# Performance work log

Measured on AMD Instinct MI355X. Metric: run time of the kernel, lower is better.

Reference implementation:

```python
import jax, jax.numpy as jnp
import numpy as np

EPS = 1e-5  # BatchNorm eps (eval mode, uses running stats)


def _conv1x1(x, W, b):
    # x: [B,C,H,W], W: [O,C], b: [O] -> [B,O,H,W]
    return jnp.einsum('bchw,oc->bohw', x, W) + b[None, :, None, None]


def setup_inputs() -> dict:
    key = jax.random.key(0)
    ks = jax.random.split(key, 13)
    B, C, M, N = 16, 512, 64, 64
    CR = C // 2
    s = 0.02
    return {
        'x': jax.random.normal(ks[0], (B, C, M, N), dtype=jnp.float32),
        'Wq': jax.random.normal(ks[1], (CR, C), dtype=jnp.float32) * s,
        'bq': jax.random.normal(ks[2], (CR,), dtype=jnp.float32) * s,
        'Wk': jax.random.normal(ks[3], (CR, C), dtype=jnp.float32) * s,
        'bk': jax.random.normal(ks[4], (CR,), dtype=jnp.float32) * s,
        'Wv': jax.random.normal(ks[5], (CR, C), dtype=jnp.float32) * s,
        'bv': jax.random.normal(ks[6], (CR,), dtype=jnp.float32) * s,
        'Wr': jax.random.normal(ks[7], (C, CR), dtype=jnp.float32) * s,
        'br': jax.random.normal(ks[8], (C,), dtype=jnp.float32) * s,
        'gamma': jax.random.normal(ks[9], (C,), dtype=jnp.float32) * 0.1 + 1.0,
        'beta': jax.random.normal(ks[10], (C,), dtype=jnp.float32) * 0.1,
        'running_mean': jax.random.normal(ks[11], (C,), dtype=jnp.float32) * 0.1,
        'running_var': jax.random.uniform(ks[12], (C,), dtype=jnp.float32, minval=0.5, maxval=1.5),
    }


def reference(x, Wq, bq, Wk, bk, Wv, bv, Wr, br, gamma, beta, running_mean, running_var):
    b, c, m, n = x.shape
    cr = Wq.shape[0]
    # 1x1-conv QKV projections
    Q = _conv1x1(x, Wq, bq).reshape(b * cr, m, n)
    K = _conv1x1(x, Wk, bk).reshape(b * cr, m, n)
    V = _conv1x1(x, Wv, bv).reshape(b * cr, m, n)
    # per-channel spatial attention over rows: [b*cr, m, m]
    corr = jnp.einsum('gik,gjk->gij', Q, K)
    attn = jax.nn.softmax(corr, axis=-1)
    y = jnp.einsum('gij,gjn->gin', attn, V).reshape(b, cr, m, n)
    # reconstruct: 1x1 conv + BatchNorm (eval mode) + residual
    y = _conv1x1(y, Wr, br)
    inv = gamma / jnp.sqrt(running_var + EPS)
    y = y * inv[None, :, None, None] + (beta - running_mean * inv)[None, :, None, None]
    return y + x
```

## Files before the change

### kernel.cpp

```cpp
#include <hip/hip_runtime.h>

typedef __attribute__((ext_vector_type(8))) short bf16x8;
typedef __attribute__((ext_vector_type(4))) float f32x4;

#define DEVI static __device__ __forceinline__

DEVI unsigned short f2b(float f) {
  union { float f; unsigned u; } v; v.f = f;
  unsigned r = v.u + 0x7fffu + ((v.u >> 16) & 1u);
  return (unsigned short)(r >> 16);
}

typedef const __attribute__((address_space(1))) void* gas1_t;
typedef __attribute__((address_space(3))) void* las3_t;
#define GL16(g, l) __builtin_amdgcn_global_load_lds((gas1_t)(g), (las3_t)(l), 16, 0, 0)

#define WAITVM(N) asm volatile("s_waitcnt vmcnt(" #N ")" ::: "memory")
#define WAITLGKM  asm volatile("s_waitcnt lgkmcnt(0)" ::: "memory")
#define SCHEDBAR  __builtin_amdgcn_sched_barrier(0)

#define OFF_WQKV  0ull
#define OFF_WR    786432ull
#define OFF_BQKV  1048576ull
#define OFF_SCALE 1051648ull
#define OFF_OFF2  1053696ull
#define OFF_XT    2097152ull
#define OFF_YT    2097152ull
#define OFF_Y     35651584ull
#define OFF_Q     69206016ull

__global__ __launch_bounds__(256) void k_xt(
    const float* __restrict__ x, unsigned short* __restrict__ xt,
    const float* __restrict__ Wq, const float* __restrict__ bq,
    const float* __restrict__ Wk, const float* __restrict__ bk,
    const float* __restrict__ Wv, const float* __restrict__ bv,
    const float* __restrict__ Wr, const float* __restrict__ br,
    const float* __restrict__ gamma, const float* __restrict__ beta,
    const float* __restrict__ rm, const float* __restrict__ rv,
    unsigned short* __restrict__ wqkv, unsigned short* __restrict__ wrb,
    float* __restrict__ bqkv, float* __restrict__ scale, float* __restrict__ off2)
{
  __shared__ unsigned short tile[64][72];
  const int t = threadIdx.x;
  const int bid = blockIdx.x + blockIdx.y * 64 + blockIdx.z * 512;

  if (bid < 1536) {
    int i = bid * 256 + t;
    if (i < 768 * 512) {
      int o = i >> 9, c = i & 511;
      float v = (o < 256) ? Wq[o * 512 + c] : (o < 512 ? Wk[(o - 256) * 512 + c] : Wv[(o - 512) * 512 + c]);
      wqkv[i] = f2b(v);
    }
    if (i < 512 * 256) wrb[i] = f2b(Wr[i]);
    if (i < 768) bqkv[i] = (i < 256) ? bq[i] : (i < 512 ? bk[i - 256] : bv[i - 512]);
    if (i < 512) {
      float inv = gamma[i] * rsqrtf(rv[i] + 1e-5f);
      scale[i] = inv;
      off2[i] = (br[i] - rm[i]) * inv + beta[i];
    }
  }

  const int b = blockIdx.z, c0 = blockIdx.y * 64, s0 = blockIdx.x * 64;
  const int r = t >> 2, cc = (t & 3) * 16;
  const float* src = x + ((size_t)b * 512 + c0 + r) * 4096 + s0 + cc;
  #pragma unroll
  for (int j = 0; j < 16; j += 4) {
    float4 v = *(const float4*)(src + j);
    tile[r][cc + j + 0] = f2b(v.x);
    tile[r][cc + j + 1] = f2b(v.y);
    tile[r][cc + j + 2] = f2b(v.z);
    tile[r][cc + j + 3] = f2b(v.w);
  }
  __syncthreads();
  unsigned short* dst = xt + ((size_t)b * 4096 + s0 + r) * 512 + c0 + cc;
  bf16x8 o0, o1;
  #pragma unroll
  for (int j = 0; j < 8; ++j) { o0[j] = tile[cc + j][r]; o1[j] = tile[cc + 8 + j][r]; }
  *(bf16x8*)(dst) = o0;
  *(bf16x8*)(dst + 8) = o1;
}

__global__ __launch_bounds__(512, 2) void k_qkv(
    const unsigned short* __restrict__ xt, const unsigned short* __restrict__ wqkv,
    const float* __restrict__ bqkv, unsigned short* __restrict__ qkv)
{
  __shared__ unsigned short Ab[2][16384];
  __shared__ unsigned short Bb[2][16384];
  const int b = blockIdx.z, o0 = blockIdx.y * 256, s0 = blockIdx.x * 256;
  const int t = threadIdx.x, w = t >> 6, l = t & 63;
  const int wm = w >> 2, wn = w & 3, lr = l & 15;
  const int lkE = (l >> 4) * 8;
  const int swE = (lr & 7) * 8;
  const int cp = (t & 7) ^ ((t >> 3) & 7);

  const unsigned short* Ag = wqkv + (size_t)(o0 + (t >> 3)) * 512 + cp * 8;
  const unsigned short* Bg = xt + ((size_t)b * 4096 + s0 + (t >> 3)) * 512 + cp * 8;

  const f32x4 z = {0.f, 0.f, 0.f, 0.f};
  f32x4 acc[8][4];
  #pragma unroll
  for (int i = 0; i < 8; ++i)
    #pragma unroll
    for (int j = 0; j < 4; ++j) acc[i][j] = z;

#define STG4(bn, kt, ph) do { \
    GL16(Ag + (kt) * 64 + (size_t)(2 * (ph) + 0) * 64 * 512, (char*)&Ab[bn][0] + (2 * (ph) + 0) * 8192 + t * 16); \
    GL16(Ag + (kt) * 64 + (size_t)(2 * (ph) + 1) * 64 * 512, (char*)&Ab[bn][0] + (2 * (ph) + 1) * 8192 + t * 16); \
    GL16(Bg + (kt) * 64 + (size_t)(2 * (ph) + 0) * 64 * 512, (char*)&Bb[bn][0] + (2 * (ph) + 0) * 8192 + t * 16); \
    GL16(Bg + (kt) * 64 + (size_t)(2 * (ph) + 1) * 64 * 512, (char*)&Bb[bn][0] + (2 * (ph) + 1) * 8192 + t * 16); \
  } while (0)

  bf16x8 af[2][4];
#define PHASE(bn, mh, nh, LOADA) do { \
    bf16x8 bfr[2][2]; \
    _Pragma("unroll") \
    for (int kc = 0; kc < 2; ++kc) { \
      const int kidx = (kc * 32 + lkE) ^ swE; \
      if (LOADA) { \
        _Pragma("unroll") \
        for (int mi4 = 0; mi4 < 4; ++mi4) \
          af[kc][mi4] = *(const bf16x8*)(&Ab[bn][(wm * 128 + ((mh) * 4 + mi4) * 16 + lr) * 64 + kidx]); \
      } \
      _Pragma("unroll") \
      for (int ni2 = 0; ni2 < 2; ++ni2) \
        bfr[kc][ni2] = *(const bf16x8*)(&Bb[bn][(wn * 64 + ((nh) * 2 + ni2) * 16 + lr) * 64 + kidx]); \
    } \
    WAITLGKM; SCHEDBAR; \
    __builtin_amdgcn_s_setprio(1); \
    _Pragma("unroll") \
    for (int kc = 0; kc < 2; ++kc) \
      _Pragma("unroll") \
      for (int mi4 = 0; mi4 < 4; ++mi4) \
        _Pragma("unroll") \
        for (int ni2 = 0; ni2 < 2; ++ni2) \
          acc[(mh) * 4 + mi4][(nh) * 2 + ni2] = \
            __builtin_amdgcn_mfma_f32_16x16x32_bf16(af[kc][mi4], bfr[kc][ni2], acc[(mh) * 4 + mi4][(nh) * 2 + ni2], 0, 0, 0); \
    __builtin_amdgcn_s_setprio(0); \
  } while (0)

  STG4(0, 0, 0); STG4(0, 0, 1);
  #pragma unroll
  for (int kt = 0; kt < 8; ++kt) {
    const int bn = kt & 1;
    if (kt < 7) STG4(bn ^ 1, kt + 1, 0);
    if (kt == 7) { WAITVM(0); } else { WAITVM(4); }
    __builtin_amdgcn_s_barrier(); SCHEDBAR;
    PHASE(bn, 0, 0, 1);
    __builtin_amdgcn_s_barrier(); SCHEDBAR;
    if (kt < 7) STG4(bn ^ 1, kt + 1, 1);
    PHASE(bn, 0, 1, 0);
    __builtin_amdgcn_s_barrier(); SCHEDBAR;
    PHASE(bn, 1, 0, 1);
    __builtin_amdgcn_s_barrier(); SCHEDBAR;
    PHASE(bn, 1, 1, 0);
    __builtin_amdgcn_s_barrier(); SCHEDBAR;
  }

  #pragma unroll
  for (int mi = 0; mi < 8; ++mi) {
    #pragma unroll
    for (int reg = 0; reg < 4; ++reg) {
      const int o = o0 + wm * 128 + mi * 16 + (l >> 4) * 4 + reg;
      const float bias = bqkv[o];
      const size_t base = (size_t)(o >> 8) * 16777216ull + ((size_t)b * 256 + (o & 255)) * 4096;
      #pragma unroll
      for (int ni = 0; ni < 4; ++ni) {
        const int s = s0 + wn * 64 + ni * 16 + lr;
        qkv[base + s] = f2b(acc[mi][ni][reg] + bias);
      }
    }
  }
#undef STG4
#undef PHASE
}

__global__ __launch_bounds__(256) void k_attn(const unsigned short* __restrict__ qkv,
                                              unsigned short* __restrict__ yout)
{
  __shared__ unsigned short Vt[64][80];
  __shared__ unsigned short P[4][16][80];
  const int g = blockIdx.x;
  const unsigned short* qg = qkv + (size_t)g * 4096;
  const unsigned short* kg = qkv + 16777216ull + (size_t)g * 4096;
  const unsigned short* vg = qkv + 33554432ull + (size_t)g * 4096;
  const int t = threadIdx.x, w = t >> 6, l = t & 63;
  const int lr = l & 15, lk = (l >> 4) * 8;

  {
    const int j = t >> 2, c0 = (t & 3) * 16;
    bf16x8 a = *(const bf16x8*)(vg + j * 64 + c0);
    bf16x8 bb = *(const bf16x8*)(vg + j * 64 + c0 + 8);
    #pragma unroll
    for (int jj = 0; jj < 8; ++jj) { Vt[c0 + jj][j] = a[jj]; Vt[c0 + 8 + jj][j] = bb[jj]; }
  }

  const f32x4 z = {0.f, 0.f, 0.f, 0.f};
  bf16x8 qf[2];
  #pragma unroll
  for (int kc = 0; kc < 2; ++kc) qf[kc] = *(const bf16x8*)(qg + (w * 16 + lr) * 64 + kc * 32 + lk);
  f32x4 accS[4] = {z, z, z, z};
  __builtin_amdgcn_s_setprio(1);
  #pragma unroll
  for (int jt = 0; jt < 4; ++jt)
    #pragma unroll
    for (int kc = 0; kc < 2; ++kc) {
      bf16x8 kf = *(const bf16x8*)(kg + (jt * 16 + lr) * 64 + kc * 32 + lk);
      accS[jt] = __builtin_amdgcn_mfma_f32_16x16x32_bf16(qf[kc], kf, accS[jt], 0, 0, 0);
    }
  __builtin_amdgcn_s_setprio(0);

  #pragma unroll
  for (int reg = 0; reg < 4; ++reg) {
    float mx = fmaxf(fmaxf(accS[0][reg], accS[1][reg]), fmaxf(accS[2][reg], accS[3][reg]));
    #pragma unroll
    for (int m = 1; m < 16; m <<= 1) mx = fmaxf(mx, __shfl_xor(mx, m, 64));
    float e0 = __expf(accS[0][reg] - mx), e1 = __expf(accS[1][reg] - mx);
    float e2 = __expf(accS[2][reg] - mx), e3 = __expf(accS[3][reg] - mx);
    float sm = e0 + e1 + e2 + e3;
    #pragma unroll
    for (int m = 1; m < 16; m <<= 1) sm += __shfl_xor(sm, m, 64);
    const float rs = 1.f / sm;
    const int row = (l >> 4) * 4 + reg;
    P[w][row][0 * 16 + lr] = f2b(e0 * rs);
    P[w][row][1 * 16 + lr] = f2b(e1 * rs);
    P[w][row][2 * 16 + lr] = f2b(e2 * rs);
    P[w][row][3 * 16 + lr] = f2b(e3 * rs);
  }
  __syncthreads();

  bf16x8 pf[2];
  #pragma unroll
  for (int kc = 0; kc < 2; ++kc) pf[kc] = *(const bf16x8*)(&P[w][lr][kc * 32 + lk]);
  f32x4 accY[4] = {z, z, z, z};
  __builtin_amdgcn_s_setprio(1);
  #pragma unroll
  for (int nt = 0; nt < 4; ++nt)
    #pragma unroll
    for (int kc = 0; kc < 2; ++kc) {
      bf16x8 vf = *(const bf16x8*)(&Vt[nt * 16 + lr][kc * 32 + lk]);
      accY[nt] = __builtin_amdgcn_mfma_f32_16x16x32_bf16(pf[kc], vf, accY[nt], 0, 0, 0);
    }
  __builtin_amdgcn_s_setprio(0);

  unsigned short* yg = yout + (size_t)g * 4096;
  #pragma unroll
  for (int nt = 0; nt < 4; ++nt)
    #pragma unroll
    for (int reg = 0; reg < 4; ++reg) {
      const int i = w * 16 + (l >> 4) * 4 + reg;
      yg[i * 64 + nt * 16 + lr] = f2b(accY[nt][reg]);
    }
}

__global__ __launch_bounds__(256) void k_yt(const unsigned short* __restrict__ y, unsigned short* __restrict__ yt)
{
  __shared__ unsigned short tile[64][72];
  const int b = blockIdx.z, cr0 = blockIdx.y * 64, s0 = blockIdx.x * 64;
  const int t = threadIdx.x, r = t >> 2, c0 = (t & 3) * 16;
  const unsigned short* src = y + ((size_t)b * 256 + cr0 + r) * 4096 + s0 + c0;
  bf16x8 a = *(const bf16x8*)(src);
  bf16x8 bb = *(const bf16x8*)(src + 8);
  #pragma unroll
  for (int j = 0; j < 8; ++j) { tile[r][c0 + j] = a[j]; tile[r][c0 + 8 + j] = bb[j]; }
  __syncthreads();
  unsigned short* dst = yt + ((size_t)b * 4096 + s0 + r) * 256 + cr0 + c0;
  bf16x8 o0, o1;
  #pragma unroll
  for (int j = 0; j < 8; ++j) { o0[j] = tile[c0 + j][r]; o1[j] = tile[c0 + 8 + j][r]; }
  *(bf16x8*)(dst) = o0;
  *(bf16x8*)(dst + 8) = o1;
}

__global__ __launch_bounds__(256) void k_recon(
    const unsigned short* __restrict__ yt, const unsigned short* __restrict__ wrb,
    const float* __restrict__ scale, const float* __restrict__ off2,
    const float* __restrict__ x, float* __restrict__ out)
{
  __shared__ unsigned short lds[2][2][8192];
  const int b = blockIdx.z, o0 = blockIdx.y * 128, s0 = blockIdx.x * 128;
  const int t = threadIdx.x, w = t >> 6, l = t & 63;
  const int wm = w >> 1, wn = w & 1, lr = l & 15;
  const int lkE = (l >> 4) * 8;
  const int swE = (lr & 7) * 8;
  const int cp = (t & 7) ^ ((t >> 3) & 7);

  const unsigned short* Ag = wrb + (size_t)(o0 + (t >> 3)) * 256 + cp * 8;
  const unsigned short* Bg = yt + ((size_t)b * 4096 + s0 + (t >> 3)) * 256 + cp * 8;

  const f32x4 z = {0.f, 0.f, 0.f, 0.f};
  f32x4 acc[4][4];
  #pragma unroll
  for (int i = 0; i < 4; ++i)
    #pragma unroll
    for (int j = 0; j < 4; ++j) acc[i][j] = z;

#define STG_R(st, kt) do { \
    _Pragma("unroll") \
    for (int j = 0; j < 4; ++j) { \
      GL16(Ag + (kt) * 64 + j * 32 * 256, (char*)&lds[st][0][0] + j * 4096 + t * 16); \
      GL16(Bg + (kt) * 64 + j * 32 * 256, (char*)&lds[st][1][0] + j * 4096 + t * 16); \
    } \
  } while (0)

#define CMP_R(st) do { \
    const unsigned short* A  = &lds[st][0][0]; \
    const unsigned short* Bl = &lds[st][1][0]; \
    _Pragma("unroll") \
    for (int kc = 0; kc < 2; ++kc) { \
      const int kidx = (kc * 32 + lkE) ^ swE; \
      bf16x8 af[4], bfr[4]; \
      _Pragma("unroll") \
      for (int mi = 0; mi < 4; ++mi) af[mi] = *(const bf16x8*)(A + (wm * 64 + mi * 16 + lr) * 64 + kidx); \
      _Pragma("unroll") \
      for (int ni = 0; ni < 4; ++ni) bfr[ni] = *(const bf16x8*)(Bl + (wn * 64 + ni * 16 + lr) * 64 + kidx); \
      _Pragma("unroll") \
      for (int mi = 0; mi < 4; ++mi) \
        _Pragma("unroll") \
        for (int ni = 0; ni < 4; ++ni) \
          acc[mi][ni] = __builtin_amdgcn_mfma_f32_16x16x32_bf16(af[mi], bfr[ni], acc[mi][ni], 0, 0, 0); \
    } \
    WAITLGKM; SCHEDBAR; \
  } while (0)

  STG_R(0, 0); STG_R(1, 1);
  #pragma unroll
  for (int kt = 0; kt < 3; ++kt) {
    WAITVM(8);
    __builtin_amdgcn_s_barrier(); SCHEDBAR;
    CMP_R(kt & 1);
    __builtin_amdgcn_s_barrier(); SCHEDBAR;
    if (kt + 2 < 4) STG_R(kt & 1, kt + 2);
  }
  WAITVM(0);
  __builtin_amdgcn_s_barrier(); SCHEDBAR;
  CMP_R(1);

  #pragma unroll
  for (int mi = 0; mi < 4; ++mi) {
    #pragma unroll
    for (int reg = 0; reg < 4; ++reg) {
      const int o = o0 + wm * 64 + mi * 16 + (l >> 4) * 4 + reg;
      const float sc = scale[o], of = off2[o];
      const size_t base = ((size_t)b * 512 + o) * 4096;
      #pragma unroll
      for (int ni = 0; ni < 4; ++ni) {
        const int s = s0 + wn * 64 + ni * 16 + lr;
        const size_t idx = base + s;
        out[idx] = acc[mi][ni][reg] * sc + of + x[idx];
      }
    }
  }
#undef STG_R
#undef CMP_R
}

extern "C" void kernel_launch(void* const* d_in, const int* in_sizes, int n_in,
                              void* d_out, int out_size, void* d_ws, size_t ws_size,
                              hipStream_t stream)
{
  const float* x     = (const float*)d_in[0];
  const float* Wq    = (const float*)d_in[1];
  const float* bq    = (const float*)d_in[2];
  const float* Wk    = (const float*)d_in[3];
  const float* bk    = (const float*)d_in[4];
  const float* Wv    = (const float*)d_in[5];
  const float* bv    = (const float*)d_in[6];
  const float* Wr    = (const float*)d_in[7];
  const float* br    = (const float*)d_in[8];
  const float* gamma = (const float*)d_in[9];
  const float* beta  = (const float*)d_in[10];
  const float* rm    = (const float*)d_in[11];
  const float* rv    = (const float*)d_in[12];

  char* ws = (char*)d_ws;
  unsigned short* wqkv  = (unsigned short*)(ws + OFF_WQKV);
  unsigned short* wrb   = (unsigned short*)(ws + OFF_WR);
  float* bqkv  = (float*)(ws + OFF_BQKV);
  float* scale = (float*)(ws + OFF_SCALE);
  float* off2  = (float*)(ws + OFF_OFF2);
  unsigned short* xt  = (unsigned short*)(ws + OFF_XT);
  unsigned short* yt  = (unsigned short*)(ws + OFF_YT);
  unsigned short* yb  = (unsigned short*)(ws + OFF_Y);
  unsigned short* qkv = (unsigned short*)(ws + OFF_Q);
  float* out = (float*)d_out;

  hipLaunchKernelGGL(k_xt, dim3(64, 8, 16), dim3(256), 0, stream,
                     x, xt, Wq, bq, Wk, bk, Wv, bv, Wr, br, gamma, beta, rm, rv,
                     wqkv, wrb, bqkv, scale, off2);
  hipLaunchKernelGGL(k_qkv, dim3(16, 3, 16), dim3(512), 0, stream, xt, wqkv, bqkv, qkv);
  hipLaunchKernelGGL(k_attn, dim3(4096), dim3(256), 0, stream, qkv, yb);
  hipLaunchKernelGGL(k_yt, dim3(64, 4, 16), dim3(256), 0, stream, yb, yt);
  hipLaunchKernelGGL(k_recon, dim3(32, 4, 16), dim3(256), 0, stream, yt, wrb, scale, off2, x, out);
}
```

Baseline: 219.8 us.

## Split QKV GEMM staging into four quarter-loads and restructure LDS-read/MFMA phases

The QKV projection GEMM main loop now issues the next tile's global-to-LDS loads in four smaller groups spread across the four compute phases instead of two larger groups. Its LDS fragment reads are split from the MFMA blocks, with extra barriers between them, so that loads and MFMA work interleave more finely. The reconstruct GEMM's inner step now reads both k-chunks of fragments before issuing all MFMAs and drops the trailing lgkm wait. The aim is better overlap of memory traffic with matrix math. The cost is more barriers per iteration and higher register pressure.

```diff
diff --git a/kernel.cpp b/kernel.cpp
--- a/kernel.cpp
+++ b/kernel.cpp
@@ -103,28 +103,40 @@
     #pragma unroll
     for (int j = 0; j < 4; ++j) acc[i][j] = z;
 
-#define STG4(bn, kt, ph) do { \
-    GL16(Ag + (kt) * 64 + (size_t)(2 * (ph) + 0) * 64 * 512, (char*)&Ab[bn][0] + (2 * (ph) + 0) * 8192 + t * 16); \
-    GL16(Ag + (kt) * 64 + (size_t)(2 * (ph) + 1) * 64 * 512, (char*)&Ab[bn][0] + (2 * (ph) + 1) * 8192 + t * 16); \
-    GL16(Bg + (kt) * 64 + (size_t)(2 * (ph) + 0) * 64 * 512, (char*)&Bb[bn][0] + (2 * (ph) + 0) * 8192 + t * 16); \
-    GL16(Bg + (kt) * 64 + (size_t)(2 * (ph) + 1) * 64 * 512, (char*)&Bb[bn][0] + (2 * (ph) + 1) * 8192 + t * 16); \
+#define STG2(bn, kt, h) do { \
+    const int c0_ = ((h) & 1) * 2, c1_ = c0_ + 1; \
+    if ((h) < 2) { \
+      GL16(Ag + (kt) * 64 + (size_t)c0_ * 64 * 512, (char*)&Ab[bn][0] + c0_ * 8192 + t * 16); \
+      GL16(Ag + (kt) * 64 + (size_t)c1_ * 64 * 512, (char*)&Ab[bn][0] + c1_ * 8192 + t * 16); \
+    } else { \
+      GL16(Bg + (kt) * 64 + (size_t)c0_ * 64 * 512, (char*)&Bb[bn][0] + c0_ * 8192 + t * 16); \
+      GL16(Bg + (kt) * 64 + (size_t)c1_ * 64 * 512, (char*)&Bb[bn][0] + c1_ * 8192 + t * 16); \
+    } \
   } while (0)
 
   bf16x8 af[2][4];
-#define PHASE(bn, mh, nh, LOADA) do { \
-    bf16x8 bfr[2][2]; \
+
+#define READ_A(bn, mh) do { \
     _Pragma("unroll") \
     for (int kc = 0; kc < 2; ++kc) { \
       const int kidx = (kc * 32 + lkE) ^ swE; \
-      if (LOADA) { \
-        _Pragma("unroll") \
-        for (int mi4 = 0; mi4 < 4; ++mi4) \
-          af[kc][mi4] = *(const bf16x8*)(&Ab[bn][(wm * 128 + ((mh) * 4 + mi4) * 16 + lr) * 64 + kidx]); \
-      } \
+      _Pragma("unroll") \
+      for (int mi4 = 0; mi4 < 4; ++mi4) \
+        af[kc][mi4] = *(const bf16x8*)(&Ab[bn][(wm * 128 + ((mh) * 4 + mi4) * 16 + lr) * 64 + kidx]); \
+    } \
+  } while (0)
+
+#define READ_B(bn, nh, bfr) do { \
+    _Pragma("unroll") \
+    for (int kc = 0; kc < 2; ++kc) { \
+      const int kidx = (kc * 32 + lkE) ^ swE; \
       _Pragma("unroll") \
       for (int ni2 = 0; ni2 < 2; ++ni2) \
         bfr[kc][ni2] = *(const bf16x8*)(&Bb[bn][(wn * 64 + ((nh) * 2 + ni2) * 16 + lr) * 64 + kidx]); \
     } \
+  } while (0)
+
+#define MFMA_Q(mh, nh, bfr) do { \
     WAITLGKM; SCHEDBAR; \
     __builtin_amdgcn_s_setprio(1); \
     _Pragma("unroll") \
@@ -138,21 +150,32 @@
     __builtin_amdgcn_s_setprio(0); \
   } while (0)
 
-  STG4(0, 0, 0); STG4(0, 0, 1);
+  STG2(0, 0, 0); STG2(0, 0, 1); STG2(0, 0, 2); STG2(0, 0, 3);
+
   #pragma unroll
   for (int kt = 0; kt < 8; ++kt) {
     const int bn = kt & 1;
-    if (kt < 7) STG4(bn ^ 1, kt + 1, 0);
-    if (kt == 7) { WAITVM(0); } else { WAITVM(4); }
-    __builtin_amdgcn_s_barrier(); SCHEDBAR;
-    PHASE(bn, 0, 0, 1);
-    __builtin_amdgcn_s_barrier(); SCHEDBAR;
-    if (kt < 7) STG4(bn ^ 1, kt + 1, 1);
-    PHASE(bn, 0, 1, 0);
-    __builtin_amdgcn_s_barrier(); SCHEDBAR;
-    PHASE(bn, 1, 0, 1);
-    __builtin_amdgcn_s_barrier(); SCHEDBAR;
-    PHASE(bn, 1, 1, 0);
+    bf16x8 bfr[2][2];
+    if (kt < 7) STG2(bn ^ 1, kt + 1, 0);
+    if (kt == 7) { WAITVM(0); } else { WAITVM(2); }
+    __builtin_amdgcn_s_barrier(); SCHEDBAR;
+    READ_A(bn, 0); READ_B(bn, 0, bfr); SCHEDBAR;
+    MFMA_Q(0, 0, bfr);
+    __builtin_amdgcn_s_barrier(); SCHEDBAR;
+    READ_B(bn, 1, bfr); SCHEDBAR;
+    if (kt < 7) STG2(bn ^ 1, kt + 1, 1);
+    __builtin_amdgcn_s_barrier(); SCHEDBAR;
+    MFMA_Q(0, 1, bfr);
+    __builtin_amdgcn_s_barrier(); SCHEDBAR;
+    READ_A(bn, 1); READ_B(bn, 0, bfr); SCHEDBAR;
+    if (kt < 7) STG2(bn ^ 1, kt + 1, 2);
+    __builtin_amdgcn_s_barrier(); SCHEDBAR;
+    MFMA_Q(1, 0, bfr);
+    __builtin_amdgcn_s_barrier(); SCHEDBAR;
+    READ_B(bn, 1, bfr); SCHEDBAR;
+    if (kt < 7) STG2(bn ^ 1, kt + 1, 3);
+    __builtin_amdgcn_s_barrier(); SCHEDBAR;
+    MFMA_Q(1, 1, bfr);
     __builtin_amdgcn_s_barrier(); SCHEDBAR;
   }
 
@@ -170,8 +193,10 @@
       }
     }
   }
-#undef STG4
-#undef PHASE
+#undef STG2
+#undef READ_A
+#undef READ_B
+#undef MFMA_Q
 }
 
 __global__ __launch_bounds__(256) void k_attn(const unsigned short* __restrict__ qkv,
@@ -305,21 +330,22 @@
 #define CMP_R(st) do { \
     const unsigned short* A  = &lds[st][0][0]; \
     const unsigned short* Bl = &lds[st][1][0]; \
+    bf16x8 af[2][4], bfr[2][4]; \
     _Pragma("unroll") \
     for (int kc = 0; kc < 2; ++kc) { \
       const int kidx = (kc * 32 + lkE) ^ swE; \
-      bf16x8 af[4], bfr[4]; \
-      _Pragma("unroll") \
-      for (int mi = 0; mi < 4; ++mi) af[mi] = *(const bf16x8*)(A + (wm * 64 + mi * 16 + lr) * 64 + kidx); \
-      _Pragma("unroll") \
-      for (int ni = 0; ni < 4; ++ni) bfr[ni] = *(const bf16x8*)(Bl + (wn * 64 + ni * 16 + lr) * 64 + kidx); \
+      _Pragma("unroll") \
+      for (int mi = 0; mi < 4; ++mi) af[kc][mi] = *(const bf16x8*)(A + (wm * 64 + mi * 16 + lr) * 64 + kidx); \
+      _Pragma("unroll") \
+      for (int ni = 0; ni < 4; ++ni) bfr[kc][ni] = *(const bf16x8*)(Bl + (wn * 64 + ni * 16 + lr) * 64 + kidx); \
+    } \
+    _Pragma("unroll") \
+    for (int kc = 0; kc < 2; ++kc) \
       _Pragma("unroll") \
       for (int mi = 0; mi < 4; ++mi) \
         _Pragma("unroll") \
         for (int ni = 0; ni < 4; ++ni) \
-          acc[mi][ni] = __builtin_amdgcn_mfma_f32_16x16x32_bf16(af[mi], bfr[ni], acc[mi][ni], 0, 0, 0); \
-    } \
-    WAITLGKM; SCHEDBAR; \
+          acc[mi][ni] = __builtin_amdgcn_mfma_f32_16x16x32_bf16(af[kc][mi], bfr[kc][ni], acc[mi][ni], 0, 0, 0); \
   } while (0)
 
   STG_R(0, 0); STG_R(1, 1);
```

After: 214.4 us. 2.4% less time.
